# Optimization experiments

Hardware: AMD Instinct MI355X
Metric: run time of the kernel (lower is better)

## Reference

```python
import jax, jax.numpy as jnp
import numpy as np

T = 0.1  # temperature
NEG_M = 1.0


def _normalize(v):
    return v / jnp.linalg.norm(v, axis=1, keepdims=True)


def setup_inputs() -> dict:
    key = jax.random.key(0)
    k1, k2 = jax.random.split(key)
    f1 = _normalize(jax.random.normal(k1, (4096, 128), dtype=jnp.float32))
    f2 = _normalize(jax.random.normal(k2, (4096, 128), dtype=jnp.float32))
    return {"f1": f1, "f2": f2, "dd": 1}


def reference(f1, f2, dd):
    # x: [N, D] with N = 2*B; dd is unused (matches original forward)
    x = jnp.concatenate([f1, f2], axis=0)
    N = x.shape[0]
    half = N // 2
    # positive pairs: (i, i+half) and (i+half, i)
    reordered = jnp.concatenate([x[half:], x[:half]], axis=0)
    # original uses .data (detached) on the second operand
    pos = jnp.exp(jnp.sum(x * jax.lax.stop_gradient(reordered), axis=1) / T)  # [N]
    sim = jnp.matmul(x, jax.lax.stop_gradient(x.T)) / T                       # [N, N]
    diag_mask = 1.0 - jnp.eye(N, dtype=x.dtype)
    all_prob = jnp.exp(sim) * diag_mask                                        # [N, N]
    all_div = all_prob.sum(axis=1)                                             # [N]
    lnPmt = pos / all_div                                                      # P(pos)
    Pon = all_prob / all_div[:, None]
    # sum_j log(1 - P_ij) minus the positive-pair term log(1 - P_pos)
    lnPon = jnp.log1p(-Pon).sum(axis=1) - jnp.log1p(-lnPmt)                    # [N]
    lnPmtsum = jnp.log(lnPmt).sum()
    lnPonsum = lnPon.sum() * NEG_M
    loss = -(lnPmtsum + lnPonsum) / N
    return loss
```

## Files before the change

### kernel.cpp

```cpp
#include <hip/hip_runtime.h>
#include <hip/hip_bf16.h>

#define HALF 4096
#define NTOT 8192
#define D 128
#define KS2 3.79828256f

typedef __attribute__((ext_vector_type(8))) short bf16x8;
typedef __attribute__((ext_vector_type(4))) float f32x4;

__device__ __forceinline__ float wave_sum64(float v) {
#pragma unroll
    for (int m = 32; m >= 1; m >>= 1) v += __shfl_xor(v, m);
    return v;
}

__device__ __forceinline__ unsigned short tobf(float v) {
    __hip_bfloat16 b = __float2bfloat16(v);
    return *(unsigned short*)&b;
}

__global__ void cast_pos_kernel(const float* __restrict__ f1, const float* __restrict__ f2,
                                unsigned short* __restrict__ xs, float* __restrict__ spos,
                                float* __restrict__ sii2) {
    int w = (blockIdx.x * blockDim.x + threadIdx.x) >> 6;
    int l = threadIdx.x & 63;
    float2 a1 = ((const float2*)(f1 + (size_t)w * D))[l];
    float2 a2 = ((const float2*)(f2 + (size_t)w * D))[l];

    ushort2 v1, v2;
    v1.x = tobf(a1.x * KS2); v1.y = tobf(a1.y * KS2);
    v2.x = tobf(a2.x * KS2); v2.y = tobf(a2.y * KS2);

    int g = w >> 4, lrow = w & 15;
    int k = l >> 4, quad = (l >> 2) & 3, j = (l & 3) * 2;
    size_t off = ((size_t)(g * 4 + k) * 64 + quad * 16 + lrow) * 8 + j;
    *(ushort2*)(xs + off)              = v1;
    *(ushort2*)(xs + off + 256 * 2048) = v2;

    float b1x = __uint_as_float((unsigned)v1.x << 16), b1y = __uint_as_float((unsigned)v1.y << 16);
    float b2x = __uint_as_float((unsigned)v2.x << 16), b2y = __uint_as_float((unsigned)v2.y << 16);
    float s1 = b1x * b1x + b1y * b1y;
    float s2 = b2x * b2x + b2y * b2y;
    float d  = a1.x * a2.x + a1.y * a2.y;
    s1 = wave_sum64(s1); s2 = wave_sum64(s2); d = wave_sum64(d);
    if (l == 0) {
        sii2[w] = s1; sii2[w + HALF] = s2;
        float sp = d * 10.0f;
        spos[w] = sp; spos[w + HALF] = sp;
    }
}

__global__ __launch_bounds__(256, 3) void gram_kernel(const unsigned short* __restrict__ xs,
                                                      float* __restrict__ E1p) {
    const int slab = blockIdx.x;
    const int panel = blockIdx.y;
    const int t = threadIdx.x;
    const int wave = t >> 6, lane = t & 63;
    const int lrow = lane & 15, quad = lane >> 4;

    const unsigned short* ab = xs + (size_t)panel * 16 * 512 + lane * 8;
    bf16x8 af[4][4];
#pragma unroll
    for (int k = 0; k < 4; ++k)
#pragma unroll
        for (int r = 0; r < 4; ++r)
            af[k][r] = *(const bf16x8*)(ab + (r * 4 + k) * 512);

    const unsigned short* bb = xs + ((size_t)slab * 64 + wave * 2) * 2048 + lane * 8;

    bf16x8 bfr[4][2];
#pragma unroll
    for (int k = 0; k < 4; ++k)
#pragma unroll
        for (int c = 0; c < 2; ++c)
            bfr[k][c] = *(const bf16x8*)(bb + (c * 4 + k) * 512);

    f32x4 rs4[4];
#pragma unroll
    for (int r = 0; r < 4; ++r) rs4[r] = (f32x4){0.f, 0.f, 0.f, 0.f};

#pragma unroll 1
    for (int tt = 0; tt < 8; ++tt) {
        f32x4 acc[4][2];
#pragma unroll
        for (int r = 0; r < 4; ++r)
#pragma unroll
            for (int c = 0; c < 2; ++c) acc[r][c] = (f32x4){0.f, 0.f, 0.f, 0.f};

#pragma unroll
        for (int k = 0; k < 4; ++k)
#pragma unroll
            for (int r = 0; r < 4; ++r)
#pragma unroll
                for (int c = 0; c < 2; ++c)
                    acc[r][c] = __builtin_amdgcn_mfma_f32_16x16x32_bf16(af[k][r], bfr[k][c], acc[r][c], 0, 0, 0);

        if (tt < 7) {
            const unsigned short* bn = bb + (size_t)(tt + 1) * 8 * 2048;
#pragma unroll
            for (int k = 0; k < 4; ++k)
#pragma unroll
                for (int c = 0; c < 2; ++c)
                    bfr[k][c] = *(const bf16x8*)(bn + (c * 4 + k) * 512);
        }

#pragma unroll
        for (int r = 0; r < 4; ++r) {
#pragma unroll
            for (int c = 0; c < 2; ++c) {
#pragma unroll
                for (int g = 0; g < 4; ++g)
                    rs4[r][g] += __builtin_amdgcn_exp2f(acc[r][c][g]);
            }
        }
    }

    const int slot = slab * 4 + wave;
#pragma unroll
    for (int r = 0; r < 4; ++r) {
#pragma unroll
        for (int g = 0; g < 4; ++g) {
            float v = rs4[r][g];
#pragma unroll
            for (int m = 1; m <= 8; m <<= 1) v += __shfl_xor(v, m);
            if (lrow == 0)
                E1p[(size_t)slot * NTOT + panel * 64 + r * 16 + quad * 4 + g] = v;
        }
    }
}

__global__ void rowterm_kernel(const float* __restrict__ E1p, const float* __restrict__ spos,
                               const float* __restrict__ sii2, float* __restrict__ pacc) {
    int i = blockIdx.x * 256 + threadIdx.x;
    float div = 0.f;
#pragma unroll
    for (int s = 0; s < 32; ++s) div += E1p[(size_t)s * NTOT + i];
    div -= __builtin_amdgcn_exp2f(sii2[i]);
    float sp = spos[i];
    float pmt = __expf(sp) / div;
    float term = sp - __logf(div) - 1.0f - __logf(1.0f - pmt);

    term = wave_sum64(term);
    __shared__ float red[4];
    if ((threadIdx.x & 63) == 0) red[threadIdx.x >> 6] = term;
    __syncthreads();
    if (threadIdx.x == 0)
        pacc[blockIdx.x] = red[0] + red[1] + red[2] + red[3];
}

__global__ void fin_kernel(const float* __restrict__ pacc, float* __restrict__ out) {
    int t = threadIdx.x;
    float v = (t < 32) ? pacc[t] : 0.f;
    v = wave_sum64(v);
    if (t == 0) out[0] = -v * (1.0f / (float)NTOT);
}

extern "C" void kernel_launch(void* const* d_in, const int* in_sizes, int n_in,
                              void* d_out, int out_size, void* d_ws, size_t ws_size,
                              hipStream_t stream) {
    const float* f1 = (const float*)d_in[0];
    const float* f2 = (const float*)d_in[1];
    float* out = (float*)d_out;

    char* ws = (char*)d_ws;
    unsigned short* xs = (unsigned short*)ws;
    float* E1p  = (float*)(ws + (size_t)NTOT * D * 2);
    float* spos = E1p + 32 * NTOT;
    float* sii2 = spos + NTOT;
    float* pacc = sii2 + NTOT;

    cast_pos_kernel<<<1024, 256, 0, stream>>>(f1, f2, xs, spos, sii2);
    gram_kernel<<<dim3(8, 128), 256, 0, stream>>>(xs, E1p);
    rowterm_kernel<<<32, 256, 0, stream>>>(E1p, spos, sii2, pacc);
    fin_kernel<<<1, 64, 0, stream>>>(pacc, out);
}
```

Baseline: 84.91 us.

## Use persistent gram blocks with atomic work queue and fuse final reduction

The gram kernel becomes persistent: 768 blocks pull (slab, panel) tiles from a global atomic counter instead of a fixed 1024-block grid, which is meant to even out load and the tail across the CUs. The separate final-reduction kernel is dropped, and the last rowterm block finishes the sum through an atomic accumulator and a completion counter. The counters are reset in the cast kernel. In exchange, each tile costs an atomic and two block barriers, and the float atomic accumulation makes the summation order nondeterministic.

```diff
diff --git a/kernel.cpp b/kernel.cpp
--- a/kernel.cpp
+++ b/kernel.cpp
@@ -22,7 +22,9 @@
 
 __global__ void cast_pos_kernel(const float* __restrict__ f1, const float* __restrict__ f2,
                                 unsigned short* __restrict__ xs, float* __restrict__ spos,
-                                float* __restrict__ sii2) {
+                                float* __restrict__ sii2, unsigned int* __restrict__ qctr,
+                                float* __restrict__ acc, unsigned int* __restrict__ done) {
+    if (blockIdx.x == 0 && threadIdx.x == 0) { *qctr = 0u; *acc = 0.f; *done = 0u; }
     int w = (blockIdx.x * blockDim.x + threadIdx.x) >> 6;
     int l = threadIdx.x & 63;
     float2 a1 = ((const float2*)(f1 + (size_t)w * D))[l];
@@ -52,86 +54,92 @@
 }
 
 __global__ __launch_bounds__(256, 3) void gram_kernel(const unsigned short* __restrict__ xs,
-                                                      float* __restrict__ E1p) {
-    const int slab = blockIdx.x;
-    const int panel = blockIdx.y;
+                                                      float* __restrict__ E1p,
+                                                      unsigned int* __restrict__ qctr) {
     const int t = threadIdx.x;
     const int wave = t >> 6, lane = t & 63;
     const int lrow = lane & 15, quad = lane >> 4;
-
-    const unsigned short* ab = xs + (size_t)panel * 16 * 512 + lane * 8;
-    bf16x8 af[4][4];
-#pragma unroll
-    for (int k = 0; k < 4; ++k)
-#pragma unroll
-        for (int r = 0; r < 4; ++r)
-            af[k][r] = *(const bf16x8*)(ab + (r * 4 + k) * 512);
-
-    const unsigned short* bb = xs + ((size_t)slab * 64 + wave * 2) * 2048 + lane * 8;
-
-    bf16x8 bfr[4][2];
-#pragma unroll
-    for (int k = 0; k < 4; ++k)
-#pragma unroll
-        for (int c = 0; c < 2; ++c)
-            bfr[k][c] = *(const bf16x8*)(bb + (c * 4 + k) * 512);
-
-    f32x4 rs4[4];
-#pragma unroll
-    for (int r = 0; r < 4; ++r) rs4[r] = (f32x4){0.f, 0.f, 0.f, 0.f};
+    __shared__ unsigned int su;
 
 #pragma unroll 1
-    for (int tt = 0; tt < 8; ++tt) {
-        f32x4 acc[4][2];
-#pragma unroll
-        for (int r = 0; r < 4; ++r)
-#pragma unroll
-            for (int c = 0; c < 2; ++c) acc[r][c] = (f32x4){0.f, 0.f, 0.f, 0.f};
+    for (;;) {
+        __syncthreads();
+        if (t == 0) su = atomicAdd(qctr, 1u);
+        __syncthreads();
+        unsigned int u = su;
+        if (u >= 1024u) break;
+        const int slab = (int)(u >> 7);
+        const int panel = (int)(u & 127u);
 
+        const unsigned short* ab = xs + (size_t)panel * 16 * 512 + lane * 8;
+        bf16x8 af[4][4];
 #pragma unroll
         for (int k = 0; k < 4; ++k)
 #pragma unroll
             for (int r = 0; r < 4; ++r)
+                af[k][r] = *(const bf16x8*)(ab + (r * 4 + k) * 512);
+
+        const unsigned short* bb = xs + ((size_t)slab * 64 + wave * 2) * 2048 + lane * 8;
+        bf16x8 bfr[4][2];
 #pragma unroll
-                for (int c = 0; c < 2; ++c)
-                    acc[r][c] = __builtin_amdgcn_mfma_f32_16x16x32_bf16(af[k][r], bfr[k][c], acc[r][c], 0, 0, 0);
+        for (int k = 0; k < 4; ++k)
+#pragma unroll
+            for (int c = 0; c < 2; ++c)
+                bfr[k][c] = *(const bf16x8*)(bb + (c * 4 + k) * 512);
 
-        if (tt < 7) {
-            const unsigned short* bn = bb + (size_t)(tt + 1) * 8 * 2048;
+        f32x4 rs4[4];
+#pragma unroll
+        for (int r = 0; r < 4; ++r) rs4[r] = (f32x4){0.f, 0.f, 0.f, 0.f};
+
+#pragma unroll 1
+        for (int tt = 0; tt < 8; ++tt) {
+            f32x4 a2[4][2];
+#pragma unroll
+            for (int r = 0; r < 4; ++r)
+#pragma unroll
+                for (int c = 0; c < 2; ++c) a2[r][c] = (f32x4){0.f, 0.f, 0.f, 0.f};
 #pragma unroll
             for (int k = 0; k < 4; ++k)
 #pragma unroll
+                for (int r = 0; r < 4; ++r)
+#pragma unroll
+                    for (int c = 0; c < 2; ++c)
+                        a2[r][c] = __builtin_amdgcn_mfma_f32_16x16x32_bf16(af[k][r], bfr[k][c], a2[r][c], 0, 0, 0);
+            if (tt < 7) {
+                const unsigned short* bn = bb + (size_t)(tt + 1) * 8 * 2048;
+#pragma unroll
+                for (int k = 0; k < 4; ++k)
+#pragma unroll
+                    for (int c = 0; c < 2; ++c)
+                        bfr[k][c] = *(const bf16x8*)(bn + (c * 4 + k) * 512);
+            }
+#pragma unroll
+            for (int r = 0; r < 4; ++r)
+#pragma unroll
                 for (int c = 0; c < 2; ++c)
-                    bfr[k][c] = *(const bf16x8*)(bn + (c * 4 + k) * 512);
+#pragma unroll
+                    for (int g = 0; g < 4; ++g)
+                        rs4[r][g] += __builtin_amdgcn_exp2f(a2[r][c][g]);
         }
 
+        const int slot = slab * 4 + wave;
 #pragma unroll
         for (int r = 0; r < 4; ++r) {
 #pragma unroll
-            for (int c = 0; c < 2; ++c) {
+            for (int g = 0; g < 4; ++g) {
+                float v = rs4[r][g];
 #pragma unroll
-                for (int g = 0; g < 4; ++g)
-                    rs4[r][g] += __builtin_amdgcn_exp2f(acc[r][c][g]);
+                for (int m = 1; m <= 8; m <<= 1) v += __shfl_xor(v, m);
+                if (lrow == 0)
+                    E1p[(size_t)slot * NTOT + panel * 64 + r * 16 + quad * 4 + g] = v;
             }
-        }
-    }
-
-    const int slot = slab * 4 + wave;
-#pragma unroll
-    for (int r = 0; r < 4; ++r) {
-#pragma unroll
-        for (int g = 0; g < 4; ++g) {
-            float v = rs4[r][g];
-#pragma unroll
-            for (int m = 1; m <= 8; m <<= 1) v += __shfl_xor(v, m);
-            if (lrow == 0)
-                E1p[(size_t)slot * NTOT + panel * 64 + r * 16 + quad * 4 + g] = v;
         }
     }
 }
 
 __global__ void rowterm_kernel(const float* __restrict__ E1p, const float* __restrict__ spos,
-                               const float* __restrict__ sii2, float* __restrict__ pacc) {
+                               const float* __restrict__ sii2, float* __restrict__ acc,
+                               unsigned int* __restrict__ done, float* __restrict__ out) {
     int i = blockIdx.x * 256 + threadIdx.x;
     float div = 0.f;
 #pragma unroll
@@ -145,15 +153,15 @@
     __shared__ float red[4];
     if ((threadIdx.x & 63) == 0) red[threadIdx.x >> 6] = term;
     __syncthreads();
-    if (threadIdx.x == 0)
-        pacc[blockIdx.x] = red[0] + red[1] + red[2] + red[3];
-}
-
-__global__ void fin_kernel(const float* __restrict__ pacc, float* __restrict__ out) {
-    int t = threadIdx.x;
-    float v = (t < 32) ? pacc[t] : 0.f;
-    v = wave_sum64(v);
-    if (t == 0) out[0] = -v * (1.0f / (float)NTOT);
+    if (threadIdx.x == 0) {
+        atomicAdd(acc, red[0] + red[1] + red[2] + red[3]);
+        __threadfence();
+        unsigned int prev = atomicAdd(done, 1u);
+        if (prev == 31u) {
+            float total = atomicAdd(acc, 0.0f);
+            out[0] = -total * (1.0f / (float)NTOT);
+        }
+    }
 }
 
 extern "C" void kernel_launch(void* const* d_in, const int* in_sizes, int n_in,
@@ -168,10 +176,11 @@
     float* E1p  = (float*)(ws + (size_t)NTOT * D * 2);
     float* spos = E1p + 32 * NTOT;
     float* sii2 = spos + NTOT;
-    float* pacc = sii2 + NTOT;
+    float* acc  = sii2 + NTOT;
+    unsigned int* done = (unsigned int*)(acc + 1);
+    unsigned int* qctr = done + 1;
 
-    cast_pos_kernel<<<1024, 256, 0, stream>>>(f1, f2, xs, spos, sii2);
-    gram_kernel<<<dim3(8, 128), 256, 0, stream>>>(xs, E1p);
-    rowterm_kernel<<<32, 256, 0, stream>>>(E1p, spos, sii2, pacc);
-    fin_kernel<<<1, 64, 0, stream>>>(pacc, out);
+    cast_pos_kernel<<<1024, 256, 0, stream>>>(f1, f2, xs, spos, sii2, qctr, acc, done);
+    gram_kernel<<<768, 256, 0, stream>>>(xs, E1p, qctr);
+    rowterm_kernel<<<32, 256, 0, stream>>>(E1p, spos, sii2, acc, done, out);
 }
```

Result: slower. 94.59 us (+11.4%).
